# Performance work log

Measured on AMD Instinct MI355X. Metric: run time of the kernel, lower is better.

The kernel has to match this reference:

```python
import jax, jax.numpy as jnp
import numpy as np

B, S, DM = 1, 2048, 2048
H, KV, DH = 32, 8, 64
ROT, DQ = 32, 16  # rotary dims; DQ = ROT // 2
GROUPS = H // KV


def setup_inputs() -> dict:
    key = jax.random.key(0)
    ks = jax.random.split(key, 9)
    sc = 0.02
    hidden_states = jax.random.normal(ks[0], (B, S, DM), jnp.float32)
    # realistic RoPE tables: theta = pos * inv_freq, shape [1,1,S,DQ] (broadcasts over heads)
    inv_freq = 1.0 / (10000.0 ** (jnp.arange(DQ, dtype=jnp.float32) / DQ))
    ang = jnp.arange(S, dtype=jnp.float32)[:, None] * inv_freq[None, :]
    cos = jnp.cos(ang)[None, None]
    sin = jnp.sin(ang)[None, None]
    position_ids = jnp.broadcast_to(jnp.arange(S, dtype=jnp.int64 if jax.config.read('jax_enable_x64') else jnp.int32), (B, S))
    Wq = jax.random.normal(ks[1], (DM, H * DH), jnp.float32) * sc
    Wk = jax.random.normal(ks[2], (DM, KV * DH), jnp.float32) * sc
    Wv = jax.random.normal(ks[3], (DM, KV * DH), jnp.float32) * sc
    Wo = jax.random.normal(ks[4], (H * DH, DM), jnp.float32) * sc
    qkv_dim = H * DH + 2 * KV * DH
    tau_Wq = jax.random.normal(ks[5], (qkv_dim, H), jnp.float32) * sc
    tau_Wv = jax.random.normal(ks[6], (qkv_dim, H), jnp.float32) * sc
    tau_alpha = jax.random.normal(ks[7], (H,), jnp.float32)
    return {"hidden_states": hidden_states, "cos": cos, "sin": sin,
            "position_ids": position_ids, "Wq": Wq, "Wk": Wk, "Wv": Wv,
            "Wo": Wo, "tau_Wq": tau_Wq, "tau_Wv": tau_Wv, "tau_alpha": tau_alpha}


def _rope(x, cos, sin):
    # x: [B, h, S, DH]; rotate first ROT dims (half-split real/imag), interleave output
    x_rot, x_pass = x[..., :ROT], x[..., ROT:]
    xr, xi = x_rot[..., :DQ], x_rot[..., DQ:]
    out_r = xr * cos - xi * sin
    out_i = xr * sin + xi * cos
    out = jnp.stack([out_r, out_i], axis=-1).reshape(x.shape[:-1] + (ROT,))
    return jnp.concatenate([out, x_pass], axis=-1)


def reference(hidden_states, cos, sin, position_ids, Wq, Wk, Wv, Wo, tau_Wq, tau_Wv, tau_alpha):
    b, s, _ = hidden_states.shape
    q = hidden_states @ Wq                      # [B,S,H*DH]
    k = hidden_states @ Wk                      # [B,S,KV*DH]
    v = hidden_states @ Wv                      # [B,S,KV*DH]
    # tau gating: gelu(concat qkv) -> tanh projections -> position sigmoid term
    feat = jax.nn.gelu(jnp.concatenate([q, k, v], axis=-1), approximate=False)
    tok_q = jnp.tanh(feat @ tau_Wq).transpose(0, 2, 1)   # [B,H,S]
    tok_v = jnp.tanh(feat @ tau_Wv).transpose(0, 2, 1)   # [B,H,S]
    pos = position_ids.astype(hidden_states.dtype) + 1.0
    tau_pos = 1.0 + (jax.nn.sigmoid(tau_alpha[None, :, None] * jnp.log(pos)[:, None, :]) - 0.5)
    tau_q = (tok_q + tau_pos)[..., None]        # [B,H,S,1]
    tau_v = (tok_v + tau_pos)[..., None]        # [B,H,S,1]
    q = q.reshape(b, s, H, DH).transpose(0, 2, 1, 3) * tau_q   # [B,H,S,DH]
    k = k.reshape(b, s, KV, DH).transpose(0, 2, 1, 3)          # [B,KV,S,DH]
    # torch: tau_v.repeat(1,groups,1,1)[:, :KV] == first KV heads of tau_v
    v = v.reshape(b, s, KV, DH).transpose(0, 2, 1, 3) * tau_v[:, :KV]
    q = _rope(q, cos, sin)
    k = _rope(k, cos, sin)
    # GQA expand kv heads, causal SDPA
    k = jnp.repeat(k, GROUPS, axis=1)
    v = jnp.repeat(v, GROUPS, axis=1)
    scores = jnp.einsum('bhqd,bhkd->bhqk', q, k) / np.sqrt(DH).astype(np.float32)
    causal = jnp.tril(jnp.ones((s, s), dtype=bool))
    scores = jnp.where(causal, scores, jnp.finfo(scores.dtype).min)
    attn = jax.nn.softmax(scores, axis=-1)
    out = jnp.einsum('bhqk,bhkd->bhqd', attn, v)
    out = out.transpose(0, 2, 1, 3).reshape(b, s, H * DH)
    return out @ Wo
```

## Files before the change

### kernel.cpp

```cpp
#include <hip/hip_runtime.h>
#include <cmath>

typedef __bf16 bf16x8 __attribute__((ext_vector_type(8)));
typedef __bf16 bf16x4 __attribute__((ext_vector_type(4)));
typedef float f32x4 __attribute__((ext_vector_type(4)));
typedef unsigned short u16;
typedef unsigned int u32;

__device__ __forceinline__ u16 f2bf(float f) {
  union { float f; unsigned int u; } v; v.f = f;
  unsigned int u = v.u;
  return (u16)((u + 0x7FFFu + ((u >> 16) & 1u)) >> 16);
}

__device__ __forceinline__ float geluf(float x) {
  return 0.5f * x * (1.0f + erff(x * 0.7071067811865475f));
}

__device__ __forceinline__ void gl_lds16(const void* g, void* l) {
  __builtin_amdgcn_global_load_lds(
      (const __attribute__((address_space(1))) u32*)g,
      (__attribute__((address_space(3))) u32*)l, 16, 0, 0);
}

__global__ __launch_bounds__(256) void cvt_bf16(const float* __restrict__ in,
                                                u16* __restrict__ out, int n8) {
  int i = blockIdx.x * 256 + threadIdx.x;
  if (i >= n8) return;
  const float4* p = (const float4*)in + 2 * (size_t)i;
  float4 a = p[0], b = p[1];
  uint4 o;
  o.x = (unsigned)f2bf(a.x) | ((unsigned)f2bf(a.y) << 16);
  o.y = (unsigned)f2bf(a.z) | ((unsigned)f2bf(a.w) << 16);
  o.z = (unsigned)f2bf(b.x) | ((unsigned)f2bf(b.y) << 16);
  o.w = (unsigned)f2bf(b.z) | ((unsigned)f2bf(b.w) << 16);
  ((uint4*)out)[i] = o;
}

__global__ __launch_bounds__(256) void transpose_all(const float* __restrict__ Wq,
                                                     const float* __restrict__ Wk,
                                                     const float* __restrict__ Wv,
                                                     const float* __restrict__ Wo,
                                                     const float* __restrict__ tWq,
                                                     const float* __restrict__ tWv,
                                                     u16* __restrict__ WqkvT,
                                                     u16* __restrict__ WoT,
                                                     u16* __restrict__ Tt) {
  __shared__ float tile[64][65];
  int b = blockIdx.x;
  const float* in; u16* out; int R, C, bx, by;
  if (b < 1024)      { in = Wq;  out = WqkvT;                R = 2048; C = 2048; bx = b & 31; by = b >> 5; }
  else if (b < 1280) { b -= 1024; in = Wk; out = WqkvT + 2048ull * 2048; R = 2048; C = 512; bx = b & 7; by = b >> 3; }
  else if (b < 1536) { b -= 1280; in = Wv; out = WqkvT + 2560ull * 2048; R = 2048; C = 512; bx = b & 7; by = b >> 3; }
  else if (b < 2560) { b -= 1536; in = Wo; out = WoT;        R = 2048; C = 2048; bx = b & 31; by = b >> 5; }
  else if (b < 2608) { b -= 2560; in = tWq; out = Tt;               R = 3072; C = 32; bx = 0; by = b; }
  else               { b -= 2608; in = tWv; out = Tt + 32ull * 3072; R = 3072; C = 32; bx = 0; by = b; }

  const int t = threadIdx.x;
  const int r0 = by * 64, c0 = bx * 64;
  const int lr = t >> 4, lc4 = (t & 15) * 4;
#pragma unroll
  for (int p = 0; p < 4; ++p) {
    int r = p * 16 + lr;
    float4 v = {0.f, 0.f, 0.f, 0.f};
    if (c0 + lc4 < C) v = *(const float4*)(in + (size_t)(r0 + r) * C + c0 + lc4);
    tile[r][lc4] = v.x; tile[r][lc4 + 1] = v.y;
    tile[r][lc4 + 2] = v.z; tile[r][lc4 + 3] = v.w;
  }
  __syncthreads();
  const int cg = t >> 4, rr4 = (t & 15) * 4;
#pragma unroll
  for (int p = 0; p < 4; ++p) {
    int c = p * 16 + cg;
    if (c0 + c < C) {
      uint2 w;
      w.x = (u32)f2bf(tile[rr4][c])     | ((u32)f2bf(tile[rr4 + 1][c]) << 16);
      w.y = (u32)f2bf(tile[rr4 + 2][c]) | ((u32)f2bf(tile[rr4 + 3][c]) << 16);
      *(uint2*)(out + (size_t)(c0 + c) * R + r0 + rr4) = w;
    }
  }
}

template <int WR, int WC>
__global__ __launch_bounds__(256, 3) void gemm_bt(const u16* __restrict__ A,
                                                  const u16* __restrict__ Bt,
                                                  float* __restrict__ Cpart,
                                                  int M, int N, int K, int kPer) {
  constexpr int BM = WR * 64, BN = WC * 64;
  __shared__ __attribute__((aligned(16))) u16 As[BM * 64];
  __shared__ __attribute__((aligned(16))) u16 Bs[BN * 64];
  const int tid = threadIdx.x, wid = tid >> 6, lane = tid & 63;
  const int l16 = lane & 15, quad = lane >> 4;
  const int wm = (wid % WR) * 64, wn = (wid / WR) * 64;
  const int m0 = blockIdx.y * BM, n0 = blockIdx.x * BN;
  const int kIters = K >> 6;
  const int kStart = blockIdx.z * kPer;
  const int kEnd = (kStart + kPer < kIters) ? (kStart + kPer) : kIters;

  const int lrow = lane >> 3;
  const int swz = (lane & 7) ^ lrow;
  const u16* gAb = A + (size_t)m0 * K + (size_t)swz * 8;
  const u16* gBb = Bt + (size_t)n0 * K + (size_t)swz * 8;
  const int sx = l16 & 7;

  f32x4 acc[4][4] = {};
  for (int kt = kStart; kt < kEnd; ++kt) {
    __syncthreads();
    const u16* gA = gAb + (size_t)kt * 64;
    const u16* gB = gBb + (size_t)kt * 64;
#pragma unroll
    for (int j = 0; j < BM / 32; ++j) {
      int i = wid * (BM / 32) + j;
      gl_lds16(gA + (size_t)(i * 8 + lrow) * K, &As[i * 512]);
    }
#pragma unroll
    for (int j = 0; j < BN / 32; ++j) {
      int i = wid * (BN / 32) + j;
      gl_lds16(gB + (size_t)(i * 8 + lrow) * K, &Bs[i * 512]);
    }
    __syncthreads();
    bf16x8 af[4][2], bfr[4][2];
#pragma unroll
    for (int mt = 0; mt < 4; ++mt)
#pragma unroll
      for (int ks = 0; ks < 2; ++ks)
        af[mt][ks] = *(const bf16x8*)(&As[(wm + mt * 16 + l16) * 64 +
                                          (((ks * 4 + quad) ^ sx) * 8)]);
#pragma unroll
    for (int nt = 0; nt < 4; ++nt)
#pragma unroll
      for (int ks = 0; ks < 2; ++ks)
        bfr[nt][ks] = *(const bf16x8*)(&Bs[(wn + nt * 16 + l16) * 64 +
                                           (((ks * 4 + quad) ^ sx) * 8)]);
#pragma unroll
    for (int mt = 0; mt < 4; ++mt)
#pragma unroll
      for (int nt = 0; nt < 4; ++nt)
#pragma unroll
        for (int ks = 0; ks < 2; ++ks)
          acc[mt][nt] = __builtin_amdgcn_mfma_f32_16x16x32_bf16(
              af[mt][ks], bfr[nt][ks], acc[mt][nt], 0, 0, 0);
  }

  float* C = Cpart + (size_t)blockIdx.z * M * N;
#pragma unroll
  for (int mt = 0; mt < 4; ++mt)
#pragma unroll
    for (int nt = 0; nt < 4; ++nt)
#pragma unroll
      for (int r = 0; r < 4; ++r) {
        int row = m0 + wm + mt * 16 + quad * 4 + r;
        int col = n0 + wn + nt * 16 + l16;
        C[(size_t)row * N + col] = acc[mt][nt][r];
      }
}

__global__ __launch_bounds__(256) void reduce_gelu(float* __restrict__ base, int P,
                                                   int n4, u16* __restrict__ gout) {
  int i = blockIdx.x * 256 + threadIdx.x;
  if (i >= n4) return;
  size_t n = (size_t)n4 * 4;
  float4 v = ((const float4*)base)[i];
  for (int p = 1; p < P; ++p) {
    float4 w = ((const float4*)(base + (size_t)p * n))[i];
    v.x += w.x; v.y += w.y; v.z += w.z; v.w += w.w;
  }
  if (P > 1) ((float4*)base)[i] = v;
  uint2 o;
  o.x = (u32)f2bf(geluf(v.x)) | ((u32)f2bf(geluf(v.y)) << 16);
  o.y = (u32)f2bf(geluf(v.z)) | ((u32)f2bf(geluf(v.w)) << 16);
  ((uint2*)gout)[i] = o;
}

__global__ __launch_bounds__(256) void reduce_add(const float* __restrict__ base, int P,
                                                  int n4, float* __restrict__ dst) {
  int i = blockIdx.x * 256 + threadIdx.x;
  if (i >= n4) return;
  size_t n = (size_t)n4 * 4;
  float4 v = ((const float4*)base)[i];
  for (int p = 1; p < P; ++p) {
    float4 w = ((const float4*)(base + (size_t)p * n))[i];
    v.x += w.x; v.y += w.y; v.z += w.z; v.w += w.w;
  }
  ((float4*)dst)[i] = v;
}

__global__ __launch_bounds__(256) void reduce_tanh(const float* __restrict__ base, int P,
                                                   int n, float* __restrict__ tokq,
                                                   float* __restrict__ tokv) {
  int i = blockIdx.x * 256 + threadIdx.x;
  if (i >= n) return;
  float v = base[i];
  for (int p = 1; p < P; ++p) v += base[(size_t)p * n + i];
  float t = tanhf(v);
  int col = i & 63, row = i >> 6;
  if (col < 32) tokq[row * 32 + col] = t;
  else          tokv[row * 32 + (col - 32)] = t;
}

#define QSCALE 0.18033688011112042f
__global__ __launch_bounds__(256) void prep_qkv(const float* __restrict__ qkv,
                                                const float* __restrict__ tokq,
                                                const float* __restrict__ tokv,
                                                const float* __restrict__ alpha,
                                                const float* __restrict__ cosb,
                                                const float* __restrict__ sinb,
                                                const int* __restrict__ pos_ids,
                                                u16* __restrict__ Qb,
                                                u16* __restrict__ Kb,
                                                u16* __restrict__ Vt,
                                                u16* __restrict__ Vb) {
  const int s = blockIdx.x;
  const int tid = threadIdx.x;
  __shared__ float cs[16], sn[16], tq_s[32], tv_s[32];
  if (tid < 16) { cs[tid] = cosb[s * 16 + tid]; sn[tid] = sinb[s * 16 + tid]; }
  if (tid < 32) {
    float p = (float)pos_ids[s] + 1.0f;
    float sig = 1.0f / (1.0f + __expf(-alpha[tid] * logf(p)));
    float taupos = 0.5f + sig;
    tq_s[tid] = (tokq[s * 32 + tid] + taupos) * QSCALE;
    tv_s[tid] = tokv[s * 32 + tid] + taupos;
  }
  __syncthreads();
  const float* row = qkv + (size_t)s * 3072;

  for (int idx = tid; idx < 2048; idx += 256) {
    int h = idx >> 6, d = idx & 63;
    float tq = tq_s[h];
    float v;
    if (d < 32) {
      int i = d >> 1;
      float xr = row[h * 64 + i] * tq, xi = row[h * 64 + 16 + i] * tq;
      v = (d & 1) ? (xr * sn[i] + xi * cs[i]) : (xr * cs[i] - xi * sn[i]);
    } else v = row[h * 64 + d] * tq;
    Qb[((size_t)h * 2048 + s) * 64 + d] = f2bf(v);
  }
  for (int idx = tid; idx < 512; idx += 256) {
    int h = idx >> 6, d = idx & 63;
    const float* kr = row + 2048;
    float v;
    if (d < 32) {
      int i = d >> 1;
      float xr = kr[h * 64 + i], xi = kr[h * 64 + 16 + i];
      v = (d & 1) ? (xr * sn[i] + xi * cs[i]) : (xr * cs[i] - xi * sn[i]);
    } else v = kr[h * 64 + d];
    Kb[((size_t)h * 2048 + s) * 64 + d] = f2bf(v);
  }
  for (int idx = tid; idx < 512; idx += 256) {
    int h = idx >> 6, d = idx & 63;
    float v = row[2560 + h * 64 + d] * tv_s[h];
    u16 b = f2bf(v);
    if (Vb) Vb[((size_t)h * 2048 + s) * 64 + d] = b;
    else    Vt[((size_t)h * 64 + d) * 2048 + s] = b;
  }
}

__global__ __launch_bounds__(256) void vtrans(const u16* __restrict__ Vb,
                                              u16* __restrict__ Vt) {
  __shared__ u16 t[64][68];
  const int s0 = blockIdx.x * 64, h = blockIdx.y;
  const int tid = threadIdx.x;
  const u16* src = Vb + ((size_t)h * 2048 + s0) * 64;
#pragma unroll
  for (int p = 0; p < 4; ++p) {
    int v = p * 256 + tid;
    int r = v >> 4, c = (v & 15) * 4;
    uint2 w = *(const uint2*)(src + (size_t)r * 64 + c);
    t[r][c] = (u16)(w.x & 0xffff); t[r][c + 1] = (u16)(w.x >> 16);
    t[r][c + 2] = (u16)(w.y & 0xffff); t[r][c + 3] = (u16)(w.y >> 16);
  }
  __syncthreads();
  u16* dst = Vt + (size_t)h * 64 * 2048 + s0;
#pragma unroll
  for (int p = 0; p < 4; ++p) {
    int v = p * 256 + tid;
    int d = v >> 4, s = (v & 15) * 4;
    uint2 w;
    w.x = (u32)t[s][d] | ((u32)t[s + 1][d] << 16);
    w.y = (u32)t[s + 2][d] | ((u32)t[s + 3][d] << 16);
    *(uint2*)(dst + (size_t)d * 2048 + s) = w;
  }
}

__global__ __launch_bounds__(256, 3) void flash_attn(const u16* __restrict__ Qb,
                                                     const u16* __restrict__ Kb,
                                                     const u16* __restrict__ Vt,
                                                     float* __restrict__ Opart,
                                                     float* __restrict__ ml) {
  __shared__ __attribute__((aligned(16))) u16 KsB[2][4096];
  __shared__ __attribute__((aligned(16))) u16 VsB[2][4096];
  __shared__ __attribute__((aligned(16))) u16 Ps[128 * 64];
  const int e = 50 - blockIdx.x;
  const int h = blockIdx.y, kvh = h >> 2;
  int a = 0;
  while (3 * (a + 1) * (a + 2) / 2 <= e) ++a;
  const int rem = e - 3 * a * (a + 1) / 2;
  const int qb = 3 * a + rem / (a + 1);
  const int cc = rem % (a + 1);
  const int k0 = cc * 6;
  const int kvTend = 2 * qb + 2;
  const int k1 = (k0 + 6 < kvTend) ? (k0 + 6) : kvTend;
  const int pid = h * 51 + e;

  const int tid = threadIdx.x, wid = tid >> 6, lane = tid & 63;
  const int l16 = lane & 15, quad = lane >> 4;
  const int lrow = lane >> 3, swz = (lane & 7) ^ lrow, sx = l16 & 7;

  const int q0 = qb * 128 + wid * 32;
  bf16x8 qf[2][2];
#pragma unroll
  for (int mt = 0; mt < 2; ++mt)
#pragma unroll
    for (int ks = 0; ks < 2; ++ks)
      qf[mt][ks] = *(const bf16x8*)(Qb + ((size_t)h * 2048 + q0 + mt * 16 + l16) * 64 +
                                    ks * 32 + quad * 8);

  f32x4 oacc[2][4] = {};
  float mrun[2] = {-3e38f, -3e38f};
  float lrun[2] = {0.f, 0.f};

  const u16* kgb = Kb + ((size_t)kvh * 2048) * 64;
  const u16* vgb = Vt + (size_t)kvh * 64 * 2048;

#define FA_STAGE(KT, BUF)                                                         \
  {                                                                               \
    const u16* kg_ = kgb + (size_t)(KT)*64 * 64;                                  \
    const u16* vg_ = vgb + (size_t)(KT)*64;                                       \
    _Pragma("unroll") for (int j = 0; j < 2; ++j) {                               \
      int i_ = wid * 2 + j;                                                       \
      gl_lds16(kg_ + (size_t)(i_ * 8 + lrow) * 64 + swz * 8, &KsB[BUF][i_ * 512]);\
      gl_lds16(vg_ + (size_t)(i_ * 8 + lrow) * 2048 + swz * 8, &VsB[BUF][i_ * 512]);\
    }                                                                             \
  }

  FA_STAGE(k0, 0)
  for (int kt = k0; kt < k1; ++kt) {
    const int cur = (kt - k0) & 1;
    __syncthreads();
    if (kt + 1 < k1) FA_STAGE(kt + 1, cur ^ 1)
    const u16* Ks = KsB[cur];
    const u16* Vs = VsB[cur];

    f32x4 sacc[2][4] = {};
#pragma unroll
    for (int kf = 0; kf < 4; ++kf) {
      bf16x8 a0 = *(const bf16x8*)(Ks + (kf * 16 + l16) * 64 + ((quad ^ sx) << 3));
      bf16x8 a1 = *(const bf16x8*)(Ks + (kf * 16 + l16) * 64 + (((4 + quad) ^ sx) << 3));
      sacc[0][kf] = __builtin_amdgcn_mfma_f32_16x16x32_bf16(a0, qf[0][0], sacc[0][kf], 0, 0, 0);
      sacc[0][kf] = __builtin_amdgcn_mfma_f32_16x16x32_bf16(a1, qf[0][1], sacc[0][kf], 0, 0, 0);
      sacc[1][kf] = __builtin_amdgcn_mfma_f32_16x16x32_bf16(a0, qf[1][0], sacc[1][kf], 0, 0, 0);
      sacc[1][kf] = __builtin_amdgcn_mfma_f32_16x16x32_bf16(a1, qf[1][1], sacc[1][kf], 0, 0, 0);
    }

    const bool msk = (kt >= 2 * qb);
#pragma unroll
    for (int mt = 0; mt < 2; ++mt) {
      const int qg = q0 + mt * 16 + l16;
      if (msk) {
        const int kb = kt * 64 + quad * 4;
#pragma unroll
        for (int kf = 0; kf < 4; ++kf)
#pragma unroll
          for (int r = 0; r < 4; ++r)
            if (kb + kf * 16 + r > qg) sacc[mt][kf][r] = -1e9f;
      }
      f32x4 m4 = sacc[mt][0];
      m4 = __builtin_elementwise_max(m4, sacc[mt][1]);
      m4 = __builtin_elementwise_max(m4, sacc[mt][2]);
      m4 = __builtin_elementwise_max(m4, sacc[mt][3]);
      float mx = fmaxf(fmaxf(m4[0], m4[1]), fmaxf(m4[2], m4[3]));
      mx = fmaxf(mx, __shfl_xor(mx, 16));
      mx = fmaxf(mx, __shfl_xor(mx, 32));
      float mn = fmaxf(mrun[mt], mx);
      float al = __builtin_amdgcn_exp2f(mrun[mt] - mn);
      mrun[mt] = mn;
      float ps = 0.f;
      const int prow = wid * 32 + mt * 16 + l16;
      u16* prp = Ps + prow * 64 + ((quad & 1) << 2);
      const int pswz = prow & 7;
#pragma unroll
      for (int kf = 0; kf < 4; ++kf) {
        bf16x4 pk;
#pragma unroll
        for (int r = 0; r < 4; ++r) {
          float p = __builtin_amdgcn_exp2f(sacc[mt][kf][r] - mn);
          ps += p;
          pk[r] = (__bf16)p;
        }
        *(bf16x4*)(prp + (((kf * 2 + (quad >> 1)) ^ pswz) << 3)) = pk;
      }
      ps += __shfl_xor(ps, 16);
      ps += __shfl_xor(ps, 32);
      lrun[mt] = lrun[mt] * al + ps;
#pragma unroll
      for (int df = 0; df < 4; ++df) oacc[mt][df] *= al;
    }

#pragma unroll
    for (int ks = 0; ks < 2; ++ks) {
      const int q0r = wid * 32 + l16, q1r = q0r + 16;
      bf16x8 b0 = *(const bf16x8*)(Ps + q0r * 64 + (((ks * 4 + quad) ^ (q0r & 7)) << 3));
      bf16x8 b1 = *(const bf16x8*)(Ps + q1r * 64 + (((ks * 4 + quad) ^ (q1r & 7)) << 3));
#pragma unroll
      for (int df = 0; df < 4; ++df) {
        bf16x8 va = *(const bf16x8*)(Vs + (df * 16 + l16) * 64 + (((ks * 4 + quad) ^ sx) << 3));
        oacc[0][df] = __builtin_amdgcn_mfma_f32_16x16x32_bf16(va, b0, oacc[0][df], 0, 0, 0);
        oacc[1][df] = __builtin_amdgcn_mfma_f32_16x16x32_bf16(va, b1, oacc[1][df], 0, 0, 0);
      }
    }
  }
#undef FA_STAGE

  float* Op = Opart + (size_t)pid * 128 * 64;
#pragma unroll
  for (int mt = 0; mt < 2; ++mt) {
    const int qrow = wid * 32 + mt * 16 + l16;
#pragma unroll
    for (int df = 0; df < 4; ++df)
      *(f32x4*)(Op + (size_t)qrow * 64 + df * 16 + quad * 4) = oacc[mt][df];
    if (quad == 0) {
      ml[((size_t)pid * 128 + qrow) * 2] = mrun[mt];
      ml[((size_t)pid * 128 + qrow) * 2 + 1] = lrun[mt];
    }
  }
}

__global__ __launch_bounds__(256) void fa_combine(const float* __restrict__ Opart,
                                                  const float* __restrict__ ml,
                                                  u16* __restrict__ Ob) {
  const int qb = blockIdx.x, h = blockIdx.y;
  const int C = (2 * qb + 7) / 6;
  const int aa = qb / 3, bb = qb % 3;
  const int base = h * 51 + 3 * aa * (aa + 1) / 2 + bb * (aa + 1);
  const int t = threadIdx.x;
#pragma unroll
  for (int u = 0; u < 8; ++u) {
    int unit = u * 256 + t;
    int row = unit >> 4, d4 = unit & 15;
    float mstar = -3e38f;
    for (int c = 0; c < C; ++c)
      mstar = fmaxf(mstar, ml[((size_t)(base + c) * 128 + row) * 2]);
    float4 o = {0.f, 0.f, 0.f, 0.f};
    float lsum = 0.f;
    for (int c = 0; c < C; ++c) {
      const float* mlp = &ml[((size_t)(base + c) * 128 + row) * 2];
      float w = __builtin_amdgcn_exp2f(mlp[0] - mstar);
      float4 v = ((const float4*)(Opart + ((size_t)(base + c) * 128 + row) * 64))[d4];
      o.x += w * v.x; o.y += w * v.y; o.z += w * v.z; o.w += w * v.w;
      lsum += w * mlp[1];
    }
    float inv = 1.0f / lsum;
    uint2 pk;
    pk.x = (u32)f2bf(o.x * inv) | ((u32)f2bf(o.y * inv) << 16);
    pk.y = (u32)f2bf(o.z * inv) | ((u32)f2bf(o.w * inv) << 16);
    *(uint2*)(Ob + (size_t)(qb * 128 + row) * 2048 + h * 64 + d4 * 4) = pk;
  }
}

extern "C" void kernel_launch(void* const* d_in, const int* in_sizes, int n_in,
                              void* d_out, int out_size, void* d_ws, size_t ws_size,
                              hipStream_t stream) {
  (void)in_sizes; (void)n_in; (void)out_size;
  const float* hidden = (const float*)d_in[0];
  const float* cosb   = (const float*)d_in[1];
  const float* sinb   = (const float*)d_in[2];
  const int*   pos    = (const int*)d_in[3];
  const float* Wq     = (const float*)d_in[4];
  const float* Wk     = (const float*)d_in[5];
  const float* Wv     = (const float*)d_in[6];
  const float* Wo     = (const float*)d_in[7];
  const float* tWq    = (const float*)d_in[8];
  const float* tWv    = (const float*)d_in[9];
  const float* alpha  = (const float*)d_in[10];
  float* out = (float*)d_out;

  const bool big = ws_size >= (size_t)120 * 1024 * 1024;
  const int Pq = big ? 2 : 1;
  const int Pt = big ? 16 : 1;
  const int Po = big ? 3 : 1;

  char* ws = (char*)d_ws;
  size_t off = 0;
  auto alloc = [&](size_t bytes) -> void* {
    void* p = ws + off;
    off += (bytes + 255) & ~(size_t)255;
    return p;
  };
  u16*   WoT   = (u16*)alloc(2048ull * 2048 * 2);
  u16*   Tt    = (u16*)alloc(64ull * 3072 * 2);
  u16*   Qb    = (u16*)alloc(32ull * 2048 * 64 * 2);
  u16*   Kb    = (u16*)alloc(8ull * 2048 * 64 * 2);
  u16*   Vt    = (u16*)alloc(8ull * 64 * 2048 * 2);
  u16*   Ob    = (u16*)alloc(2048ull * 2048 * 2);
  u16*   featb = (u16*)alloc(2048ull * 3072 * 2);
  float* tokq  = (float*)alloc(2048ull * 32 * 4);
  float* tokv  = (float*)alloc(2048ull * 32 * 4);
  u16*   Vb    = big ? (u16*)alloc(8ull * 2048 * 64 * 2) : nullptr;
  size_t E = off;
  u16*   Xb      = (u16*)alloc(2048ull * 2048 * 2);
  u16*   WqkvT   = (u16*)alloc(3072ull * 2048 * 2);
  float* qkvPart = (float*)alloc((size_t)Pq * 2048 * 3072 * 4);
  float* qkv     = qkvPart;
  float* tokPart = (float*)(ws + E);
  float* Opart   = (float*)(ws + E);
  float* mlbuf   = (float*)(ws + E + 1632ull * 128 * 64 * 4);
  float* outPart = (float*)(ws + E);

  cvt_bf16<<<2048, 256, 0, stream>>>(hidden, Xb, 2048 * 2048 / 8);
  transpose_all<<<2656, 256, 0, stream>>>(Wq, Wk, Wv, Wo, tWq, tWv, WqkvT, WoT, Tt);

  gemm_bt<2, 2><<<dim3(24, 16, Pq), 256, 0, stream>>>(
      Xb, WqkvT, qkvPart, 2048, 3072, 2048, (32 + Pq - 1) / Pq);
  reduce_gelu<<<6144, 256, 0, stream>>>(qkvPart, Pq, 2048 * 3072 / 4, featb);

  gemm_bt<4, 1><<<dim3(1, 8, Pt), 256, 0, stream>>>(
      featb, Tt, tokPart, 2048, 64, 3072, (48 + Pt - 1) / Pt);
  reduce_tanh<<<512, 256, 0, stream>>>(tokPart, Pt, 2048 * 64, tokq, tokv);

  prep_qkv<<<2048, 256, 0, stream>>>(qkv, tokq, tokv, alpha, cosb, sinb, pos,
                                     Qb, Kb, Vt, Vb);
  if (big) vtrans<<<dim3(32, 8), 256, 0, stream>>>(Vb, Vt);

  flash_attn<<<dim3(51, 32), 256, 0, stream>>>(Qb, Kb, Vt, Opart, mlbuf);
  fa_combine<<<dim3(16, 32), 256, 0, stream>>>(Opart, mlbuf, Ob);

  gemm_bt<2, 2><<<dim3(16, 16, Po), 256, 0, stream>>>(
      Ob, WoT, outPart, 2048, 2048, 2048, (32 + Po - 1) / Po);
  reduce_add<<<4096, 256, 0, stream>>>(outPart, Po, 2048 * 2048 / 4, out);
}
```

Baseline: 288.5 us.

## Fuse setup kernels, fold tanh reduce into prep, atomic split-K output, bf16 partials

Merges the hidden-state bf16 conversion into the weight-transpose kernel, folds the tanh split-K reduction into prep_qkv, and stores flash-attention partial outputs as bf16 instead of fp32. The output projection's split-K now accumulates directly into the output with float atomics after a memset, which removes the separate reduce_add pass. The intent is fewer launches and less intermediate memory traffic. In exchange it adds atomic contention, nondeterministic summation order and some precision loss in the attention partials.

```diff
diff --git a/kernel.cpp b/kernel.cpp
--- a/kernel.cpp
+++ b/kernel.cpp
@@ -12,6 +12,9 @@
   unsigned int u = v.u;
   return (u16)((u + 0x7FFFu + ((u >> 16) & 1u)) >> 16);
 }
+__device__ __forceinline__ float bf2f(u16 b) {
+  union { u32 u; float f; } v; v.u = ((u32)b) << 16; return v.f;
+}
 
 __device__ __forceinline__ float geluf(float x) {
   return 0.5f * x * (1.0f + erff(x * 0.7071067811865475f));
@@ -23,31 +26,32 @@
       (__attribute__((address_space(3))) u32*)l, 16, 0, 0);
 }
 
-__global__ __launch_bounds__(256) void cvt_bf16(const float* __restrict__ in,
-                                                u16* __restrict__ out, int n8) {
-  int i = blockIdx.x * 256 + threadIdx.x;
-  if (i >= n8) return;
-  const float4* p = (const float4*)in + 2 * (size_t)i;
-  float4 a = p[0], b = p[1];
-  uint4 o;
-  o.x = (unsigned)f2bf(a.x) | ((unsigned)f2bf(a.y) << 16);
-  o.y = (unsigned)f2bf(a.z) | ((unsigned)f2bf(a.w) << 16);
-  o.z = (unsigned)f2bf(b.x) | ((unsigned)f2bf(b.y) << 16);
-  o.w = (unsigned)f2bf(b.z) | ((unsigned)f2bf(b.w) << 16);
-  ((uint4*)out)[i] = o;
-}
-
-__global__ __launch_bounds__(256) void transpose_all(const float* __restrict__ Wq,
-                                                     const float* __restrict__ Wk,
-                                                     const float* __restrict__ Wv,
-                                                     const float* __restrict__ Wo,
-                                                     const float* __restrict__ tWq,
-                                                     const float* __restrict__ tWv,
-                                                     u16* __restrict__ WqkvT,
-                                                     u16* __restrict__ WoT,
-                                                     u16* __restrict__ Tt) {
+__global__ __launch_bounds__(256) void setup_all(const float* __restrict__ hidden,
+                                                 const float* __restrict__ Wq,
+                                                 const float* __restrict__ Wk,
+                                                 const float* __restrict__ Wv,
+                                                 const float* __restrict__ Wo,
+                                                 const float* __restrict__ tWq,
+                                                 const float* __restrict__ tWv,
+                                                 u16* __restrict__ Xb,
+                                                 u16* __restrict__ WqkvT,
+                                                 u16* __restrict__ WoT,
+                                                 u16* __restrict__ Tt) {
   __shared__ float tile[64][65];
   int b = blockIdx.x;
+  if (b < 2048) {
+    int i = b * 256 + threadIdx.x;
+    const float4* p = (const float4*)hidden + 2 * (size_t)i;
+    float4 a = p[0], c = p[1];
+    uint4 o;
+    o.x = (u32)f2bf(a.x) | ((u32)f2bf(a.y) << 16);
+    o.y = (u32)f2bf(a.z) | ((u32)f2bf(a.w) << 16);
+    o.z = (u32)f2bf(c.x) | ((u32)f2bf(c.y) << 16);
+    o.w = (u32)f2bf(c.z) | ((u32)f2bf(c.w) << 16);
+    ((uint4*)Xb)[i] = o;
+    return;
+  }
+  b -= 2048;
   const float* in; u16* out; int R, C, bx, by;
   if (b < 1024)      { in = Wq;  out = WqkvT;                R = 2048; C = 2048; bx = b & 31; by = b >> 5; }
   else if (b < 1280) { b -= 1024; in = Wk; out = WqkvT + 2048ull * 2048; R = 2048; C = 512; bx = b & 7; by = b >> 3; }
@@ -81,7 +85,7 @@
   }
 }
 
-template <int WR, int WC>
+template <int WR, int WC, bool ATOMIC>
 __global__ __launch_bounds__(256, 3) void gemm_bt(const u16* __restrict__ A,
                                                   const u16* __restrict__ Bt,
                                                   float* __restrict__ Cpart,
@@ -142,7 +146,7 @@
               af[mt][ks], bfr[nt][ks], acc[mt][nt], 0, 0, 0);
   }
 
-  float* C = Cpart + (size_t)blockIdx.z * M * N;
+  float* C = ATOMIC ? Cpart : Cpart + (size_t)blockIdx.z * M * N;
 #pragma unroll
   for (int mt = 0; mt < 4; ++mt)
 #pragma unroll
@@ -151,7 +155,10 @@
       for (int r = 0; r < 4; ++r) {
         int row = m0 + wm + mt * 16 + quad * 4 + r;
         int col = n0 + wn + nt * 16 + l16;
-        C[(size_t)row * N + col] = acc[mt][nt][r];
+        if constexpr (ATOMIC)
+          unsafeAtomicAdd(&C[(size_t)row * N + col], acc[mt][nt][r]);
+        else
+          C[(size_t)row * N + col] = acc[mt][nt][r];
       }
 }
 
@@ -172,36 +179,10 @@
   ((uint2*)gout)[i] = o;
 }
 
-__global__ __launch_bounds__(256) void reduce_add(const float* __restrict__ base, int P,
-                                                  int n4, float* __restrict__ dst) {
-  int i = blockIdx.x * 256 + threadIdx.x;
-  if (i >= n4) return;
-  size_t n = (size_t)n4 * 4;
-  float4 v = ((const float4*)base)[i];
-  for (int p = 1; p < P; ++p) {
-    float4 w = ((const float4*)(base + (size_t)p * n))[i];
-    v.x += w.x; v.y += w.y; v.z += w.z; v.w += w.w;
-  }
-  ((float4*)dst)[i] = v;
-}
-
-__global__ __launch_bounds__(256) void reduce_tanh(const float* __restrict__ base, int P,
-                                                   int n, float* __restrict__ tokq,
-                                                   float* __restrict__ tokv) {
-  int i = blockIdx.x * 256 + threadIdx.x;
-  if (i >= n) return;
-  float v = base[i];
-  for (int p = 1; p < P; ++p) v += base[(size_t)p * n + i];
-  float t = tanhf(v);
-  int col = i & 63, row = i >> 6;
-  if (col < 32) tokq[row * 32 + col] = t;
-  else          tokv[row * 32 + (col - 32)] = t;
-}
-
 #define QSCALE 0.18033688011112042f
 __global__ __launch_bounds__(256) void prep_qkv(const float* __restrict__ qkv,
-                                                const float* __restrict__ tokq,
-                                                const float* __restrict__ tokv,
+                                                const float* __restrict__ tokPart,
+                                                int P,
                                                 const float* __restrict__ alpha,
                                                 const float* __restrict__ cosb,
                                                 const float* __restrict__ sinb,
@@ -212,14 +193,21 @@
                                                 u16* __restrict__ Vb) {
   const int s = blockIdx.x;
   const int tid = threadIdx.x;
-  __shared__ float cs[16], sn[16], tq_s[32], tv_s[32];
+  __shared__ float cs[16], sn[16], tk[64], tq_s[32], tv_s[32];
   if (tid < 16) { cs[tid] = cosb[s * 16 + tid]; sn[tid] = sinb[s * 16 + tid]; }
+  if (tid >= 64 && tid < 128) {
+    int c = tid - 64;
+    float v = 0.f;
+    for (int p = 0; p < P; ++p) v += tokPart[(size_t)p * 2048 * 64 + s * 64 + c];
+    tk[c] = tanhf(v);
+  }
+  __syncthreads();
   if (tid < 32) {
     float p = (float)pos_ids[s] + 1.0f;
     float sig = 1.0f / (1.0f + __expf(-alpha[tid] * logf(p)));
     float taupos = 0.5f + sig;
-    tq_s[tid] = (tokq[s * 32 + tid] + taupos) * QSCALE;
-    tv_s[tid] = tokv[s * 32 + tid] + taupos;
+    tq_s[tid] = (tk[tid] + taupos) * QSCALE;
+    tv_s[tid] = tk[tid + 32] + taupos;
   }
   __syncthreads();
   const float* row = qkv + (size_t)s * 3072;
@@ -285,7 +273,7 @@
 __global__ __launch_bounds__(256, 3) void flash_attn(const u16* __restrict__ Qb,
                                                      const u16* __restrict__ Kb,
                                                      const u16* __restrict__ Vt,
-                                                     float* __restrict__ Opart,
+                                                     u16* __restrict__ Opart,
                                                      float* __restrict__ ml) {
   __shared__ __attribute__((aligned(16))) u16 KsB[2][4096];
   __shared__ __attribute__((aligned(16))) u16 VsB[2][4096];
@@ -411,13 +399,17 @@
   }
 #undef FA_STAGE
 
-  float* Op = Opart + (size_t)pid * 128 * 64;
+  u16* Op = Opart + (size_t)pid * 128 * 64;
 #pragma unroll
   for (int mt = 0; mt < 2; ++mt) {
     const int qrow = wid * 32 + mt * 16 + l16;
 #pragma unroll
-    for (int df = 0; df < 4; ++df)
-      *(f32x4*)(Op + (size_t)qrow * 64 + df * 16 + quad * 4) = oacc[mt][df];
+    for (int df = 0; df < 4; ++df) {
+      uint2 pk;
+      pk.x = (u32)f2bf(oacc[mt][df][0]) | ((u32)f2bf(oacc[mt][df][1]) << 16);
+      pk.y = (u32)f2bf(oacc[mt][df][2]) | ((u32)f2bf(oacc[mt][df][3]) << 16);
+      *(uint2*)(Op + (size_t)qrow * 64 + df * 16 + quad * 4) = pk;
+    }
     if (quad == 0) {
       ml[((size_t)pid * 128 + qrow) * 2] = mrun[mt];
       ml[((size_t)pid * 128 + qrow) * 2 + 1] = lrun[mt];
@@ -425,7 +417,7 @@
   }
 }
 
-__global__ __launch_bounds__(256) void fa_combine(const float* __restrict__ Opart,
+__global__ __launch_bounds__(256) void fa_combine(const u16* __restrict__ Opart,
                                                   const float* __restrict__ ml,
                                                   u16* __restrict__ Ob) {
   const int qb = blockIdx.x, h = blockIdx.y;
@@ -445,8 +437,9 @@
     for (int c = 0; c < C; ++c) {
       const float* mlp = &ml[((size_t)(base + c) * 128 + row) * 2];
       float w = __builtin_amdgcn_exp2f(mlp[0] - mstar);
-      float4 v = ((const float4*)(Opart + ((size_t)(base + c) * 128 + row) * 64))[d4];
-      o.x += w * v.x; o.y += w * v.y; o.z += w * v.z; o.w += w * v.w;
+      uint2 v = *(const uint2*)(Opart + ((size_t)(base + c) * 128 + row) * 64 + d4 * 4);
+      o.x += w * bf2f((u16)(v.x & 0xffff)); o.y += w * bf2f((u16)(v.x >> 16));
+      o.z += w * bf2f((u16)(v.y & 0xffff)); o.w += w * bf2f((u16)(v.y >> 16));
       lsum += w * mlp[1];
     }
     float inv = 1.0f / lsum;
@@ -493,8 +486,6 @@
   u16*   Vt    = (u16*)alloc(8ull * 64 * 2048 * 2);
   u16*   Ob    = (u16*)alloc(2048ull * 2048 * 2);
   u16*   featb = (u16*)alloc(2048ull * 3072 * 2);
-  float* tokq  = (float*)alloc(2048ull * 32 * 4);
-  float* tokv  = (float*)alloc(2048ull * 32 * 4);
   u16*   Vb    = big ? (u16*)alloc(8ull * 2048 * 64 * 2) : nullptr;
   size_t E = off;
   u16*   Xb      = (u16*)alloc(2048ull * 2048 * 2);
@@ -502,29 +493,27 @@
   float* qkvPart = (float*)alloc((size_t)Pq * 2048 * 3072 * 4);
   float* qkv     = qkvPart;
   float* tokPart = (float*)(ws + E);
-  float* Opart   = (float*)(ws + E);
-  float* mlbuf   = (float*)(ws + E + 1632ull * 128 * 64 * 4);
-  float* outPart = (float*)(ws + E);
-
-  cvt_bf16<<<2048, 256, 0, stream>>>(hidden, Xb, 2048 * 2048 / 8);
-  transpose_all<<<2656, 256, 0, stream>>>(Wq, Wk, Wv, Wo, tWq, tWv, WqkvT, WoT, Tt);
-
-  gemm_bt<2, 2><<<dim3(24, 16, Pq), 256, 0, stream>>>(
+  u16*   Opart   = (u16*)(ws + E);
+  float* mlbuf   = (float*)(ws + E + 1632ull * 128 * 64 * 2);
+
+  setup_all<<<4704, 256, 0, stream>>>(hidden, Wq, Wk, Wv, Wo, tWq, tWv,
+                                      Xb, WqkvT, WoT, Tt);
+
+  gemm_bt<2, 2, false><<<dim3(24, 16, Pq), 256, 0, stream>>>(
       Xb, WqkvT, qkvPart, 2048, 3072, 2048, (32 + Pq - 1) / Pq);
   reduce_gelu<<<6144, 256, 0, stream>>>(qkvPart, Pq, 2048 * 3072 / 4, featb);
 
-  gemm_bt<4, 1><<<dim3(1, 8, Pt), 256, 0, stream>>>(
+  gemm_bt<4, 1, false><<<dim3(1, 8, Pt), 256, 0, stream>>>(
       featb, Tt, tokPart, 2048, 64, 3072, (48 + Pt - 1) / Pt);
-  reduce_tanh<<<512, 256, 0, stream>>>(tokPart, Pt, 2048 * 64, tokq, tokv);
-
-  prep_qkv<<<2048, 256, 0, stream>>>(qkv, tokq, tokv, alpha, cosb, sinb, pos,
+
+  prep_qkv<<<2048, 256, 0, stream>>>(qkv, tokPart, Pt, alpha, cosb, sinb, pos,
                                      Qb, Kb, Vt, Vb);
   if (big) vtrans<<<dim3(32, 8), 256, 0, stream>>>(Vb, Vt);
 
   flash_attn<<<dim3(51, 32), 256, 0, stream>>>(Qb, Kb, Vt, Opart, mlbuf);
   fa_combine<<<dim3(16, 32), 256, 0, stream>>>(Opart, mlbuf, Ob);
 
-  gemm_bt<2, 2><<<dim3(16, 16, Po), 256, 0, stream>>>(
-      Ob, WoT, outPart, 2048, 2048, 2048, (32 + Po - 1) / Po);
-  reduce_add<<<4096, 256, 0, stream>>>(outPart, Po, 2048 * 2048 / 4, out);
-}
+  hipMemsetAsync(out, 0, 2048ull * 2048 * 4, stream);
+  gemm_bt<2, 2, true><<<dim3(16, 16, Po), 256, 0, stream>>>(
+      Ob, WoT, out, 2048, 2048, 2048, (32 + Po - 1) / Po);
+}
```

Result: slower. 317.4 us (+10.0%).
